# Kernel tuning notes

Measured on AMD Instinct MI355X. Metric: run time of the kernel, lower is better.

## Reference

```python
import jax, jax.numpy as jnp
import numpy as np

INIT_SCALE = 1.0
TEMPERATURE = 0.6
EPS_NOISE = 1e-4  # eps_noise in segment_max_hot


def setup_inputs() -> dict:
    key = jax.random.key(0)
    k1, k2, k3, k4 = jax.random.split(key, 4)
    E = 20_000_000        # number of edges / candidate logits
    n_groups = 1_000_000  # number of segments (nodes)
    logits = jax.random.normal(k1, (E,), dtype=jnp.float32)
    logit_groups = jnp.sort(jax.random.randint(k2, (E,), 0, n_groups, dtype=jnp.int32))
    # uniforms clamped away from {0,1} so -log(-log(u)) is finite
    u_gumbel = jax.random.uniform(k3, (E,), dtype=jnp.float32, minval=1e-6, maxval=1.0 - 1e-6)
    u_eps = jax.random.uniform(k4, (E,), dtype=jnp.float32, minval=0.0, maxval=1.0)
    return {"logits": logits, "logit_groups": logit_groups, "n_groups": n_groups,
            "u_gumbel": u_gumbel, "u_eps": u_eps}


def reference(logits, logit_groups, n_groups, u_gumbel, u_eps):
    # Gumbel(0, scale) sample via inverse CDF: g = -scale * log(-log(u))
    g = -INIT_SCALE * jnp.log(-jnp.log(u_gumbel))
    s = (g + logits) / TEMPERATURE
    # segment_softmax: numerically stable per-segment softmax
    smax = jax.ops.segment_max(s, logit_groups, num_segments=n_groups)
    e = jnp.exp(s - smax[logit_groups])
    denom = jax.ops.segment_sum(e, logit_groups, num_segments=n_groups)
    soft = e / denom[logit_groups]
    # segment_max_hot: tiny noise breaks ties, mark per-segment argmax as 1
    sn = soft + EPS_NOISE * u_eps
    m = jax.ops.segment_max(sn, logit_groups, num_segments=n_groups)
    s_hot = (sn == m[logit_groups]).astype(jnp.int32)
    hot_f = s_hot.astype(jnp.float32)
    # straight-through: hard one-hot forward, soft gradient
    st = soft + jax.lax.stop_gradient(hot_f - soft)
    return st, s_hot, soft
```

## Files before the change

kernel.cpp:

```cpp
#include <hip/hip_runtime.h>
#include <math.h>


#define TEMP 0.6f
#define EPS  1.0e-4f

#define BLOCK 256
#define GPB   256
#define CAP   6400

__global__ void starts_kernel(const int* __restrict__ groups, int* __restrict__ starts,
                              int E, int n_groups) {
  int i = blockIdx.x * blockDim.x + threadIdx.x;
  if (i > E) return;
  int gcur  = (i < E) ? groups[i] : n_groups;
  int gprev = (i > 0) ? groups[i - 1] : -1;
  for (int g = gprev + 1; g <= gcur; ++g) starts[g] = i;
}

__device__ __forceinline__ int lower_bound(const int* __restrict__ groups, int E, int target) {
  int lo = 0, hi = E;
  while (lo < hi) {
    int mid = (lo + hi) >> 1;
    if (groups[mid] < target) lo = mid + 1; else hi = mid;
  }
  return lo;
}

__device__ void process_group_global(const float* __restrict__ logits,
                                     const float* __restrict__ ug,
                                     const float* __restrict__ ue,
                                     int s0, int s1,
                                     float* __restrict__ o_st,
                                     float* __restrict__ o_hot,
                                     float* __restrict__ o_soft) {
  float smax = -INFINITY;
  for (int i = s0; i < s1; ++i) {
    float gm = -logf(-logf(ug[i]));
    smax = fmaxf(smax, (gm + logits[i]) / TEMP);
  }
  float denom = 0.0f;
  for (int i = s0; i < s1; ++i) {
    float gm = -logf(-logf(ug[i]));
    denom += expf((gm + logits[i]) / TEMP - smax);
  }
  float m = -INFINITY;
  for (int i = s0; i < s1; ++i) {
    float gm = -logf(-logf(ug[i]));
    float soft = expf((gm + logits[i]) / TEMP - smax) / denom;
    float sn = __fadd_rn(soft, __fmul_rn(EPS, ue[i]));
    m = fmaxf(m, sn);
  }
  for (int i = s0; i < s1; ++i) {
    float gm = -logf(-logf(ug[i]));
    float soft = expf((gm + logits[i]) / TEMP - smax) / denom;
    float sn = __fadd_rn(soft, __fmul_rn(EPS, ue[i]));
    float hot = (sn == m) ? 1.0f : 0.0f;
    o_st[i]   = __fadd_rn(soft, __fsub_rn(hot, soft));
    o_hot[i]  = hot;
    o_soft[i] = soft;
  }
}

__global__ void __launch_bounds__(BLOCK)
gumbel_fused(const float* __restrict__ logits,
             const float* __restrict__ ug,
             const float* __restrict__ ue,
             const int*   __restrict__ starts,
             float* __restrict__ o_st,
             float* __restrict__ o_hot,
             float* __restrict__ o_soft,
             int n_groups) {
  __shared__ float         sh_s[CAP];
  __shared__ unsigned char sh_g[CAP];
  __shared__ float         sh_smax[GPB];
  __shared__ float         sh_den[GPB];
  __shared__ unsigned int  sh_m[GPB];

  const int tid = threadIdx.x;
  const int g0  = blockIdx.x * GPB;
  if (g0 >= n_groups) return;
  const int gEnd = min(g0 + GPB, n_groups);

  const int A  = starts[g0];
  const int B  = starts[gEnd];
  const int nE = B - A;

  const int g = g0 + tid;
  int s0 = 0, s1 = 0;
  if (g < gEnd) { s0 = starts[g]; s1 = starts[g + 1]; }

  if (nE <= CAP) {
    sh_m[tid] = 0u;
    for (int i = A + tid; i < B; i += BLOCK) {
      float gm = -logf(-logf(ug[i]));
      sh_s[i - A] = (gm + logits[i]) / TEMP;
    }
    __syncthreads();

    float smax = -INFINITY;
    for (int i = s0; i < s1; ++i) smax = fmaxf(smax, sh_s[i - A]);
    float denom = 0.0f;
    for (int i = s0; i < s1; ++i) {
      denom += expf(sh_s[i - A] - smax);
      sh_g[i - A] = (unsigned char)tid;
    }
    sh_smax[tid] = smax;
    sh_den[tid]  = denom;
    __syncthreads();

    for (int i = A + tid; i < B; i += BLOCK) {
      int   lg   = sh_g[i - A];
      float e    = expf(sh_s[i - A] - sh_smax[lg]);
      float soft = e / sh_den[lg];
      sh_s[i - A] = soft;
      float sn = __fadd_rn(soft, __fmul_rn(EPS, ue[i]));
      atomicMax(&sh_m[lg], __float_as_uint(sn));
    }
    __syncthreads();

    for (int i = A + tid; i < B; i += BLOCK) {
      int   lg   = sh_g[i - A];
      float soft = sh_s[i - A];
      float sn   = __fadd_rn(soft, __fmul_rn(EPS, ue[i]));
      float m    = __uint_as_float(sh_m[lg]);
      float hot  = (sn == m) ? 1.0f : 0.0f;
      o_st[i]   = __fadd_rn(soft, __fsub_rn(hot, soft));
      o_hot[i]  = hot;
      o_soft[i] = soft;
    }
  } else {
    if (g < gEnd && s1 > s0)
      process_group_global(logits, ug, ue, s0, s1, o_st, o_hot, o_soft);
  }
}

__global__ void gumbel_nows(const float* __restrict__ logits,
                            const int*   __restrict__ groups,
                            const float* __restrict__ ug,
                            const float* __restrict__ ue,
                            float* __restrict__ o_st,
                            float* __restrict__ o_hot,
                            float* __restrict__ o_soft,
                            int E, int n_groups) {
  int g = blockIdx.x * blockDim.x + threadIdx.x;
  if (g >= n_groups) return;
  int s0 = lower_bound(groups, E, g);
  int s1 = lower_bound(groups, E, g + 1);
  if (s1 > s0)
    process_group_global(logits, ug, ue, s0, s1, o_st, o_hot, o_soft);
}

extern "C" void kernel_launch(void* const* d_in, const int* in_sizes, int n_in,
                              void* d_out, int out_size, void* d_ws, size_t ws_size,
                              hipStream_t stream) {
  const float* logits   = (const float*)d_in[0];
  const int*   groups   = (const int*)  d_in[1];
  const float* u_gumbel = (const float*)d_in[3];
  const float* u_eps    = (const float*)d_in[4];
  const int E        = in_sizes[0];
  const int n_groups = 1000000;

  float* out_st   = (float*)d_out;
  float* out_hot  = out_st  + E;
  float* out_soft = out_hot + E;

  size_t need = (size_t)(n_groups + 1) * sizeof(int);
  if (ws_size >= need) {
    int* starts = (int*)d_ws;
    int thr = E + 1;
    starts_kernel<<<(thr + 255) / 256, 256, 0, stream>>>(groups, starts, E, n_groups);
    int blocks = (n_groups + GPB - 1) / GPB;
    gumbel_fused<<<blocks, BLOCK, 0, stream>>>(logits, u_gumbel, u_eps, starts,
                                               out_st, out_hot, out_soft, n_groups);
  } else {
    gumbel_nows<<<(n_groups + 255) / 256, 256, 0, stream>>>(
        logits, groups, u_gumbel, u_eps, out_st, out_hot, out_soft, E, n_groups);
  }
}
```

Baseline: 518.8 us.

## Compute segment max via shared atomics and parallel exp, add nontemporal stores

Replaces the per-thread serial segment-max and exp loop with a coalesced pass that reads group ids and does shared-memory atomicMax on order-preserving float keys. Exponentials are then computed element-parallel, so each thread only sums precomputed values serially. Output stores become nontemporal and the soft output is written earlier. In exchange the kernel reads the group array again, adds an extra barrier and shared atomics, and lowers CAP so more groups fall back to the slow global path.

```diff
diff --git a/kernel.cpp b/kernel.cpp
--- a/kernel.cpp
+++ b/kernel.cpp
@@ -7,7 +7,7 @@
 
 #define BLOCK 256
 #define GPB   256
-#define CAP   6400
+#define CAP   5760
 
 __global__ void starts_kernel(const int* __restrict__ groups, int* __restrict__ starts,
                               int E, int n_groups) {
@@ -62,8 +62,18 @@
   }
 }
 
+__device__ __forceinline__ unsigned int float_key(float f) {
+  unsigned int b = __float_as_uint(f);
+  return b ^ ((unsigned int)((int)b >> 31) | 0x80000000u);
+}
+__device__ __forceinline__ float key_float(unsigned int k) {
+  unsigned int dec = (k & 0x80000000u) ? (k ^ 0x80000000u) : ~k;
+  return __uint_as_float(dec);
+}
+
 __global__ void __launch_bounds__(BLOCK)
 gumbel_fused(const float* __restrict__ logits,
+             const int*   __restrict__ groups,
              const float* __restrict__ ug,
              const float* __restrict__ ue,
              const int*   __restrict__ starts,
@@ -73,7 +83,7 @@
              int n_groups) {
   __shared__ float         sh_s[CAP];
   __shared__ unsigned char sh_g[CAP];
-  __shared__ float         sh_smax[GPB];
+  __shared__ unsigned int  sh_smax[GPB];
   __shared__ float         sh_den[GPB];
   __shared__ unsigned int  sh_m[GPB];
 
@@ -91,29 +101,37 @@
   if (g < gEnd) { s0 = starts[g]; s1 = starts[g + 1]; }
 
   if (nE <= CAP) {
-    sh_m[tid] = 0u;
+    sh_smax[tid] = 0u;
+    sh_m[tid]    = 0u;
+    __syncthreads();
+
     for (int i = A + tid; i < B; i += BLOCK) {
       float gm = -logf(-logf(ug[i]));
-      sh_s[i - A] = (gm + logits[i]) / TEMP;
+      float s  = (gm + logits[i]) / TEMP;
+      int   lg = groups[i] - g0;
+      sh_s[i - A] = s;
+      sh_g[i - A] = (unsigned char)lg;
+      atomicMax(&sh_smax[lg], float_key(s));
     }
-    __syncthreads();
-
-    float smax = -INFINITY;
-    for (int i = s0; i < s1; ++i) smax = fmaxf(smax, sh_s[i - A]);
-    float denom = 0.0f;
-    for (int i = s0; i < s1; ++i) {
-      denom += expf(sh_s[i - A] - smax);
-      sh_g[i - A] = (unsigned char)tid;
-    }
-    sh_smax[tid] = smax;
-    sh_den[tid]  = denom;
     __syncthreads();
 
     for (int i = A + tid; i < B; i += BLOCK) {
       int   lg   = sh_g[i - A];
-      float e    = expf(sh_s[i - A] - sh_smax[lg]);
-      float soft = e / sh_den[lg];
+      float smax = key_float(sh_smax[lg]);
+      sh_s[i - A] = expf(sh_s[i - A] - smax);
+    }
+    __syncthreads();
+
+    float denom = 0.0f;
+    for (int i = s0; i < s1; ++i) denom += sh_s[i - A];
+    sh_den[tid] = denom;
+    __syncthreads();
+
+    for (int i = A + tid; i < B; i += BLOCK) {
+      int   lg   = sh_g[i - A];
+      float soft = sh_s[i - A] / sh_den[lg];
       sh_s[i - A] = soft;
+      __builtin_nontemporal_store(soft, &o_soft[i]);
       float sn = __fadd_rn(soft, __fmul_rn(EPS, ue[i]));
       atomicMax(&sh_m[lg], __float_as_uint(sn));
     }
@@ -125,9 +143,8 @@
       float sn   = __fadd_rn(soft, __fmul_rn(EPS, ue[i]));
       float m    = __uint_as_float(sh_m[lg]);
       float hot  = (sn == m) ? 1.0f : 0.0f;
-      o_st[i]   = __fadd_rn(soft, __fsub_rn(hot, soft));
-      o_hot[i]  = hot;
-      o_soft[i] = soft;
+      __builtin_nontemporal_store(__fadd_rn(soft, __fsub_rn(hot, soft)), &o_st[i]);
+      __builtin_nontemporal_store(hot, &o_hot[i]);
     }
   } else {
     if (g < gEnd && s1 > s0)
@@ -171,7 +188,7 @@
     int thr = E + 1;
     starts_kernel<<<(thr + 255) / 256, 256, 0, stream>>>(groups, starts, E, n_groups);
     int blocks = (n_groups + GPB - 1) / GPB;
-    gumbel_fused<<<blocks, BLOCK, 0, stream>>>(logits, u_gumbel, u_eps, starts,
+    gumbel_fused<<<blocks, BLOCK, 0, stream>>>(logits, groups, u_gumbel, u_eps, starts,
                                                out_st, out_hot, out_soft, n_groups);
   } else {
     gumbel_nows<<<(n_groups + 255) / 256, 256, 0, stream>>>(
```

New measurement: 552.2 us. +6.4%, slower.

## Store exps in shared memory, reload group ids from global, and raise occupancy

Applied to the files above, without the earlier changes.

The per-thread denominator loop now writes exp(s - smax) back into shared memory, so the block-wide pass only divides by the group denominator and no longer recomputes the exponential. The per-element shared byte array of group ids and the shared smax array are removed; group ids are re-read from the global groups array. This shrinks shared memory per block (CAP also reduced) and the launch bounds request 6 blocks per SM to raise occupancy. Soft output is written earlier, and the strided loops are unrolled by 2 or 4. The cost is extra global reads of groups, and more blocks fall back to the slow per-thread global path because of the smaller CAP.

```diff
diff --git a/kernel.cpp b/kernel.cpp
--- a/kernel.cpp
+++ b/kernel.cpp
@@ -7,7 +7,7 @@
 
 #define BLOCK 256
 #define GPB   256
-#define CAP   6400
+#define CAP   5760
 
 __global__ void starts_kernel(const int* __restrict__ groups, int* __restrict__ starts,
                               int E, int n_groups) {
@@ -62,8 +62,9 @@
   }
 }
 
-__global__ void __launch_bounds__(BLOCK)
+__global__ void __launch_bounds__(BLOCK, 6)
 gumbel_fused(const float* __restrict__ logits,
+             const int*   __restrict__ groups,
              const float* __restrict__ ug,
              const float* __restrict__ ue,
              const int*   __restrict__ starts,
@@ -71,11 +72,9 @@
              float* __restrict__ o_hot,
              float* __restrict__ o_soft,
              int n_groups) {
-  __shared__ float         sh_s[CAP];
-  __shared__ unsigned char sh_g[CAP];
-  __shared__ float         sh_smax[GPB];
-  __shared__ float         sh_den[GPB];
-  __shared__ unsigned int  sh_m[GPB];
+  __shared__ float        sh_s[CAP];
+  __shared__ float        sh_den[GPB];
+  __shared__ unsigned int sh_m[GPB];
 
   const int tid = threadIdx.x;
   const int g0  = blockIdx.x * GPB;
@@ -92,9 +91,16 @@
 
   if (nE <= CAP) {
     sh_m[tid] = 0u;
-    for (int i = A + tid; i < B; i += BLOCK) {
-      float gm = -logf(-logf(ug[i]));
-      sh_s[i - A] = (gm + logits[i]) / TEMP;
+
+    for (int i = A + tid; i < B; i += 4 * BLOCK) {
+      #pragma unroll
+      for (int j = 0; j < 4; ++j) {
+        int ii = i + j * BLOCK;
+        if (ii < B) {
+          float gm = -logf(-logf(ug[ii]));
+          sh_s[ii - A] = (gm + logits[ii]) / TEMP;
+        }
+      }
     }
     __syncthreads();
 
@@ -102,32 +108,43 @@
     for (int i = s0; i < s1; ++i) smax = fmaxf(smax, sh_s[i - A]);
     float denom = 0.0f;
     for (int i = s0; i < s1; ++i) {
-      denom += expf(sh_s[i - A] - smax);
-      sh_g[i - A] = (unsigned char)tid;
+      float e = expf(sh_s[i - A] - smax);
+      denom += e;
+      sh_s[i - A] = e;
     }
-    sh_smax[tid] = smax;
-    sh_den[tid]  = denom;
+    sh_den[tid] = denom;
     __syncthreads();
 
-    for (int i = A + tid; i < B; i += BLOCK) {
-      int   lg   = sh_g[i - A];
-      float e    = expf(sh_s[i - A] - sh_smax[lg]);
-      float soft = e / sh_den[lg];
-      sh_s[i - A] = soft;
-      float sn = __fadd_rn(soft, __fmul_rn(EPS, ue[i]));
-      atomicMax(&sh_m[lg], __float_as_uint(sn));
+    for (int i = A + tid; i < B; i += 2 * BLOCK) {
+      #pragma unroll
+      for (int j = 0; j < 2; ++j) {
+        int ii = i + j * BLOCK;
+        if (ii < B) {
+          int   lg   = groups[ii] - g0;
+          float soft = sh_s[ii - A] / sh_den[lg];
+          sh_s[ii - A] = soft;
+          o_soft[ii]   = soft;
+          float sn = __fadd_rn(soft, __fmul_rn(EPS, ue[ii]));
+          atomicMax(&sh_m[lg], __float_as_uint(sn));
+        }
+      }
     }
     __syncthreads();
 
-    for (int i = A + tid; i < B; i += BLOCK) {
-      int   lg   = sh_g[i - A];
-      float soft = sh_s[i - A];
-      float sn   = __fadd_rn(soft, __fmul_rn(EPS, ue[i]));
-      float m    = __uint_as_float(sh_m[lg]);
-      float hot  = (sn == m) ? 1.0f : 0.0f;
-      o_st[i]   = __fadd_rn(soft, __fsub_rn(hot, soft));
-      o_hot[i]  = hot;
-      o_soft[i] = soft;
+    for (int i = A + tid; i < B; i += 4 * BLOCK) {
+      #pragma unroll
+      for (int j = 0; j < 4; ++j) {
+        int ii = i + j * BLOCK;
+        if (ii < B) {
+          int   lg   = groups[ii] - g0;
+          float soft = sh_s[ii - A];
+          float sn   = __fadd_rn(soft, __fmul_rn(EPS, ue[ii]));
+          float m    = __uint_as_float(sh_m[lg]);
+          float hot  = (sn == m) ? 1.0f : 0.0f;
+          o_st[ii]  = __fadd_rn(soft, __fsub_rn(hot, soft));
+          o_hot[ii] = hot;
+        }
+      }
     }
   } else {
     if (g < gEnd && s1 > s0)
@@ -171,7 +188,7 @@
     int thr = E + 1;
     starts_kernel<<<(thr + 255) / 256, 256, 0, stream>>>(groups, starts, E, n_groups);
     int blocks = (n_groups + GPB - 1) / GPB;
-    gumbel_fused<<<blocks, BLOCK, 0, stream>>>(logits, u_gumbel, u_eps, starts,
+    gumbel_fused<<<blocks, BLOCK, 0, stream>>>(logits, groups, u_gumbel, u_eps, starts,
                                                out_st, out_hot, out_soft, n_groups);
   } else {
     gumbel_nows<<<(n_groups + 255) / 256, 256, 0, stream>>>(
```

Measured after the change: 540.3 us. 1.04x slower.
